# Performance work log

Measured on AMD Instinct MI355X. Metric: run time of the kernel, lower is better.

The kernel has to match this reference:

```python
import jax, jax.numpy as jnp
import numpy as np

B, T, R = 64, 256, 256          # batch, timepoints, n_rois (T==R required by bmm path)
H, NH, DH, FF, LAT, L = 256, 8, 32, 512, 64, 2
EPS = 1e-5


def layernorm(x, g, b):
    m = x.mean(-1, keepdims=True)
    v = ((x - m) ** 2).mean(-1, keepdims=True)
    return (x - m) / jnp.sqrt(v + EPS) * g + b


def leaky_relu(x):
    return jnp.where(x >= 0, x, 0.1 * x)


def setup_inputs() -> dict:
    key = jax.random.key(0)
    ks = iter(jax.random.split(key, 64))
    def nrm(shape, s=0.02):
        return jax.random.normal(next(ks), shape, jnp.float32) * s
    return {
        "x": jax.random.normal(next(ks), (B, T, R), jnp.float32),
        "node_view": jax.random.normal(next(ks), (B, R, R), jnp.float32) * 0.1,
        "edge_view": jax.random.normal(next(ks), (B, R, R), jnp.float32) * 0.1,
        "fp_w": nrm((H, R)), "fp_b": jnp.zeros((H,)),
        "fp_g": jnp.ones((H,)), "fp_beta": jnp.zeros((H,)),
        "qkv_w": nrm((L, 3 * H, H)), "qkv_b": jnp.zeros((L, 3 * H)),
        "attn_out_w": nrm((L, H, H)), "attn_out_b": jnp.zeros((L, H)),
        "ln1_g": jnp.ones((L, H)), "ln1_b": jnp.zeros((L, H)),
        "ff1_w": nrm((L, FF, H)), "ff1_b": jnp.zeros((L, FF)),
        "ff2_w": nrm((L, H, FF)), "ff2_b": jnp.zeros((L, H)),
        "ln2_g": jnp.ones((L, H)), "ln2_b": jnp.zeros((L, H)),
        "out_w": nrm((R, H)), "out_b": jnp.zeros((R,)),
        "mu_w1": nrm((H // 2, H)), "mu_b1": jnp.zeros((H // 2,)),
        "mu_g": jnp.ones((H // 2,)), "mu_beta": jnp.zeros((H // 2,)),
        "mu_w2": nrm((LAT, H // 2)), "mu_b2": jnp.zeros((LAT,)),
        "lv_w1": nrm((H // 2, H)), "lv_b1": jnp.zeros((H // 2,)),
        "lv_g": jnp.ones((H // 2,)), "lv_beta": jnp.zeros((H // 2,)),
        "lv_w2": nrm((LAT, H // 2)), "lv_b2": jnp.zeros((LAT,)),
    }


def reference(x, node_view, edge_view, fp_w, fp_b, fp_g, fp_beta,
              qkv_w, qkv_b, attn_out_w, attn_out_b, ln1_g, ln1_b,
              ff1_w, ff1_b, ff2_w, ff2_b, ln2_g, ln2_b,
              out_w, out_b, mu_w1, mu_b1, mu_g, mu_beta, mu_w2, mu_b2,
              lv_w1, lv_b1, lv_g, lv_beta, lv_w2, lv_b2):
    # graph-view message passing: bmm(x^T, view), averaged, transposed back
    xr = jnp.swapaxes(x, 1, 2)                           # [B,R,T]
    msg = 0.5 * (jnp.einsum('brt,btq->brq', xr, node_view)
                 + jnp.einsum('brt,btq->brq', xr, edge_view))
    h = jnp.swapaxes(msg, 1, 2)                          # [B,T,R]
    # feature_proj: Linear -> LayerNorm -> LeakyReLU(0.1) -> Dropout(eval)
    h = leaky_relu(layernorm(h @ fp_w.T + fp_b, fp_g, fp_beta))  # [B,T,H]
    # TransformerEncoder (post-norm, relu FFN, dropout=identity)
    scale = 1.0 / jnp.sqrt(jnp.float32(DH))
    for i in range(L):
        qkv = h @ qkv_w[i].T + qkv_b[i]                  # [B,T,3H]
        q, k, v = jnp.split(qkv, 3, axis=-1)
        q = q.reshape(B, T, NH, DH).transpose(0, 2, 1, 3)
        k = k.reshape(B, T, NH, DH).transpose(0, 2, 1, 3)
        v = v.reshape(B, T, NH, DH).transpose(0, 2, 1, 3)
        attn = jax.nn.softmax(jnp.einsum('bhqd,bhkd->bhqk', q, k) * scale, axis=-1)
        o = jnp.einsum('bhqk,bhkd->bhqd', attn, v).transpose(0, 2, 1, 3).reshape(B, T, H)
        o = o @ attn_out_w[i].T + attn_out_b[i]
        h = layernorm(h + o, ln1_g[i], ln1_b[i])
        f = jax.nn.relu(h @ ff1_w[i].T + ff1_b[i]) @ ff2_w[i].T + ff2_b[i]
        h = layernorm(h + f, ln2_g[i], ln2_b[i])
    # fresh linear (treated as fixed params) then batched Pearson correlation
    y = h @ out_w.T + out_b                              # [B,T,R]
    data = jnp.swapaxes(y, 1, 2)                         # [B,R,T]
    c = data - data.mean(-1, keepdims=True)
    std = jnp.sqrt((c ** 2).sum(-1, keepdims=True) / (T - 1))   # unbiased, like torch.std
    cn = c / (std + 1e-8)
    corr = jnp.einsum('brt,bst->brs', cn, cn) / (T - 1)
    corr = jnp.nan_to_num(jnp.clip(corr, -1.0, 1.0), nan=0.0)   # [B,R,R]
    # heads
    pooled = h.mean(axis=1)                              # [B,H]
    mu = leaky_relu(layernorm(pooled @ mu_w1.T + mu_b1, mu_g, mu_beta)) @ mu_w2.T + mu_b2
    logvar = leaky_relu(layernorm(pooled @ lv_w1.T + lv_b1, lv_g, lv_beta)) @ lv_w2.T + lv_b2
    return mu, logvar, corr
```

## Files before the change

### kernel.cpp

```cpp
#include <hip/hip_runtime.h>
#include <hip/hip_bf16.h>
#include <math.h>

#define BB 64
#define NLAYER 2

typedef __attribute__((ext_vector_type(8))) short bfrag;
typedef __attribute__((ext_vector_type(4))) float f4_t;

__device__ __forceinline__ float dot4(float4 a, float4 b, float acc) {
    acc = fmaf(a.x, b.x, acc);
    acc = fmaf(a.y, b.y, acc);
    acc = fmaf(a.z, b.z, acc);
    acc = fmaf(a.w, b.w, acc);
    return acc;
}

__device__ __forceinline__ ushort f2bf(float f) {
    uint32_t u = __float_as_uint(f);
    uint32_t r = (u + 0x7FFFu + ((u >> 16) & 1u)) >> 16;
    return (ushort)r;
}
__device__ __forceinline__ float bf2f(ushort u) {
    return __uint_as_float(((uint32_t)u) << 16);
}

__device__ __forceinline__ void gll16(const ushort* g, ushort* l) {
    __builtin_amdgcn_global_load_lds(
        (const __attribute__((address_space(1))) void*)g,
        (__attribute__((address_space(3))) void*)l, 16, 0, 0);
}

__global__ __launch_bounds__(256) void k_cvt(
    const float* __restrict__ fp_w, const float* __restrict__ qkv_w,
    const float* __restrict__ aow, const float* __restrict__ f1w,
    const float* __restrict__ f2w, const float* __restrict__ outw,
    ushort* __restrict__ dst) {
    const int g = blockIdx.x;
    const size_t idx = (size_t)g * 2048 + threadIdx.x * 8;
    const float* src;
    size_t base;
    if (g < 32)       { src = fp_w;  base = 0; }
    else if (g < 224) { src = qkv_w; base = 65536; }
    else if (g < 288) { src = aow;   base = 458752; }
    else if (g < 416) { src = f1w;   base = 589824; }
    else if (g < 544) { src = f2w;   base = 851968; }
    else              { src = outw;  base = 1114112; }
    const float4* s4 = reinterpret_cast<const float4*>(src + (idx - base));
    float4 a = s4[0], b = s4[1];
    bfrag o;
    o[0] = (short)f2bf(a.x); o[1] = (short)f2bf(a.y);
    o[2] = (short)f2bf(a.z); o[3] = (short)f2bf(a.w);
    o[4] = (short)f2bf(b.x); o[5] = (short)f2bf(b.y);
    o[6] = (short)f2bf(b.z); o[7] = (short)f2bf(b.w);
    *reinterpret_cast<bfrag*>(dst + idx) = o;
}

#define MM97_STAGE(SRC, LDS, KSTRIDE)                                        \
    {                                                                        \
        _Pragma("unroll")                                                    \
        for (int c = 0; c < 4; ++c) {                                        \
            const int rr = (w << 5) + (c << 3) + (lane >> 3);                \
            gll16(SRC + (size_t)rr * (KSTRIDE) + k0 + ((lane & 7) << 3),     \
                  LDS + (((w << 5) + (c << 3)) << 6));                       \
        }                                                                    \
    }

#define MM97_COMPUTE()                                                       \
    _Pragma("unroll")                                                        \
    for (int ks = 0; ks < 2; ++ks) {                                         \
        const int kb = ks * 32 + fq * 8;                                     \
        bfrag af[4], bfv[4];                                                 \
        _Pragma("unroll")                                                    \
        for (int fm = 0; fm < 4; ++fm)                                       \
            af[fm] = *reinterpret_cast<const bfrag*>(                        \
                &As[((wm * 64 + fm * 16 + fr) << 6) + kb]);                  \
        _Pragma("unroll")                                                    \
        for (int fn = 0; fn < 4; ++fn)                                       \
            bfv[fn] = *reinterpret_cast<const bfrag*>(                       \
                &Bs[((wn * 64 + fn * 16 + fr) << 6) + kb]);                  \
        _Pragma("unroll")                                                    \
        for (int fm = 0; fm < 4; ++fm)                                       \
            _Pragma("unroll")                                                \
            for (int fn = 0; fn < 4; ++fn)                                   \
                acc[fm][fn] = __builtin_amdgcn_mfma_f32_16x16x32_bf16(       \
                    bfv[fn], af[fm], acc[fm][fn], 0, 0, 0);                  \
    }

template <int EPI, bool WF32, bool WBF>
__global__ __launch_bounds__(256) void k_mm97(
    const ushort* __restrict__ A, const ushort* __restrict__ B,
    const float* __restrict__ bias, float* __restrict__ C,
    ushort* __restrict__ Cb, int K, int N,
    size_t aStr, size_t bStr, size_t cStr) {
    __shared__ __align__(16) ushort As[128 * 64];
    __shared__ __align__(16) ushort Bs[128 * 64];
    const int tid = threadIdx.x;
    const int m0 = blockIdx.x * 128, n0 = blockIdx.y * 128;
    const size_t z = blockIdx.z;
    const int w = tid >> 6, lane = tid & 63;
    const int wm = w >> 1, wn = w & 1;
    const int fr = lane & 15, fq = lane >> 4;

    const ushort* aB = A + z * aStr + (size_t)m0 * K;
    const ushort* bB = B + z * bStr + (size_t)n0 * K;

    f4_t acc[4][4];
#pragma unroll
    for (int i = 0; i < 4; ++i)
#pragma unroll
        for (int j = 0; j < 4; ++j) acc[i][j] = (f4_t)0.f;

    for (int k0 = 0; k0 < K; k0 += 64) {
        MM97_STAGE(aB, As, K)
        MM97_STAGE(bB, Bs, K)
        __syncthreads();
        MM97_COMPUTE()
        __syncthreads();
    }

#pragma unroll
    for (int fn = 0; fn < 4; ++fn) {
// ... 7 lines not shown
            float v0 = acc[fm][fn][0] + bv.x;
            float v1 = acc[fm][fn][1] + bv.y;
            float v2 = acc[fm][fn][2] + bv.z;
            float v3 = acc[fm][fn][3] + bv.w;
            if (EPI == 2) {
                v0 = fmaxf(v0, 0.f); v1 = fmaxf(v1, 0.f);
                v2 = fmaxf(v2, 0.f); v3 = fmaxf(v3, 0.f);
            }
            const size_t o = cStr * z + (size_t)row * N + col0;
            if (WF32) {
                float4 fv = {v0, v1, v2, v3};
                *reinterpret_cast<float4*>(&C[o]) = fv;
            }
            if (WBF) {
                ushort4 uv;
                uv.x = f2bf(v0); uv.y = f2bf(v1);
                uv.z = f2bf(v2); uv.w = f2bf(v3);
                *reinterpret_cast<ushort4*>(&Cb[o]) = uv;
            }
        }
    }
}

__global__ __launch_bounds__(256) void k_mmqkv97(
    const ushort* __restrict__ A, const ushort* __restrict__ B,
    const float* __restrict__ bias, ushort* __restrict__ qb,
    ushort* __restrict__ kbuf, ushort* __restrict__ vtb) {
    __shared__ __align__(16) ushort As[128 * 64];
    __shared__ __align__(16) ushort Bs[128 * 64];
    const int tid = threadIdx.x;
    const int m0 = blockIdx.x * 128, n0 = blockIdx.y * 128;
    const int w = tid >> 6, lane = tid & 63;
    const int wm = w >> 1, wn = w & 1;
    const int fr = lane & 15, fq = lane >> 4;
    const int K = 256;

    const ushort* aB = A + (size_t)m0 * K;
    const ushort* bB = B + (size_t)n0 * K;

    f4_t acc[4][4];
#pragma unroll
    for (int i = 0; i < 4; ++i)
#pragma unroll
        for (int j = 0; j < 4; ++j) acc[i][j] = (f4_t)0.f;

    for (int k0 = 0; k0 < K; k0 += 64) {
        MM97_STAGE(aB, As, K)
        MM97_STAGE(bB, Bs, K)
        __syncthreads();
        MM97_COMPUTE()
        __syncthreads();
    }

    const int sec = n0 >> 8;
// ... 8 lines not shown
            const int b = row >> 8, t = row & 255;
            const size_t bh = (size_t)b * 8 + hd;
            float v0 = acc[fm][fn][0] + bv.x;
            float v1 = acc[fm][fn][1] + bv.y;
            float v2 = acc[fm][fn][2] + bv.z;
            float v3 = acc[fm][fn][3] + bv.w;
            if (sec < 2) {
                ushort4 uv;
                uv.x = f2bf(v0); uv.y = f2bf(v1);
                uv.z = f2bf(v2); uv.w = f2bf(v3);
                ushort* dst = (sec == 0 ? qb : kbuf) + (bh * 256 + t) * 32 + dq;
                *reinterpret_cast<ushort4*>(dst) = uv;
            } else {
                ushort* dst = vtb + (bh * 32 + dq) * 256 + t;
                dst[0] = f2bf(v0);
                dst[256] = f2bf(v1);
                dst[512] = f2bf(v2);
                dst[768] = f2bf(v3);
            }
        }
    }
}

__global__ __launch_bounds__(256) void k_corr97(
    const ushort* __restrict__ A, const float* __restrict__ stats,
    float* __restrict__ C) {
    __shared__ __align__(16) ushort As[128 * 64];
    __shared__ __align__(16) ushort Bs[128 * 64];
    const int tid = threadIdx.x;
    const int m0 = blockIdx.x * 128, n0 = blockIdx.y * 128;
    const size_t z = blockIdx.z;
    const int w = tid >> 6, lane = tid & 63;
    const int wm = w >> 1, wn = w & 1;
    const int fr = lane & 15, fq = lane >> 4;
    const int K = 256;

    const ushort* aB = A + z * 65536 + (size_t)m0 * K;
    const ushort* bB = A + z * 65536 + (size_t)n0 * K;

    f4_t acc[4][4];
#pragma unroll
    for (int i = 0; i < 4; ++i)
#pragma unroll
        for (int j = 0; j < 4; ++j) acc[i][j] = (f4_t)0.f;

    for (int k0 = 0; k0 < K; k0 += 64) {
        MM97_STAGE(aB, As, K)
        MM97_STAGE(bB, Bs, K)
        __syncthreads();
        MM97_COMPUTE()
        __syncthreads();
    }

    const float* st = stats + z * 512;
// ... 7 lines not shown
            const int row = m0 + wm * 64 + fm * 16 + fr;
            const float mui = st[row];
            const float isi = st[256 + row] * (1.f / 255.f);
            float v0 = (acc[fm][fn][0] - 256.f * mui * muj.x) * isi * isj.x;
            float v1 = (acc[fm][fn][1] - 256.f * mui * muj.y) * isi * isj.y;
            float v2 = (acc[fm][fn][2] - 256.f * mui * muj.z) * isi * isj.z;
            float v3 = (acc[fm][fn][3] - 256.f * mui * muj.w) * isi * isj.w;
            if (v0 != v0) v0 = 0.f;
            if (v1 != v1) v1 = 0.f;
            if (v2 != v2) v2 = 0.f;
            if (v3 != v3) v3 = 0.f;
            v0 = fminf(1.f, fmaxf(-1.f, v0));
            v1 = fminf(1.f, fmaxf(-1.f, v1));
            v2 = fminf(1.f, fmaxf(-1.f, v2));
            v3 = fminf(1.f, fmaxf(-1.f, v3));
            float4 fv = {v0, v1, v2, v3};
            *reinterpret_cast<float4*>(
                &C[z * 65536 + (size_t)row * 256 + col0]) = fv;
        }
    }
}

template <int ACT, bool RES>
__global__ __launch_bounds__(256) void k_mmln(
    const ushort* __restrict__ A, const ushort* __restrict__ W,
    const float* __restrict__ bias, const ushort* __restrict__ res,
    const float* __restrict__ g, const float* __restrict__ bt,
    ushort* __restrict__ outb, int K) {
    __shared__ __align__(16) ushort As[32 * 72];
    __shared__ __align__(16) ushort Bs[256 * 72];
    __shared__ float redS[32][4];
    __shared__ float redQ[32][4];
    const int tid = threadIdx.x;
    const int m0 = blockIdx.x * 32;
    const int w = tid >> 6, lane = tid & 63;
    const int fr = lane & 15, fq = lane >> 4;

    const int arow = tid >> 3, akc = (tid & 7) * 8;
    const ushort* aS = A + (size_t)(m0 + arow) * K + akc;
    ushort* aD = &As[arow * 72 + akc];
    const int brow = tid >> 1, bkc = (tid & 1) * 32;
    const ushort* bS0 = W + (size_t)brow * K + bkc;
    const ushort* bS1 = W + (size_t)(brow + 128) * K + bkc;
    ushort* bD0 = &Bs[brow * 72 + bkc];
    ushort* bD1 = &Bs[(brow + 128) * 72 + bkc];

    f4_t acc[2][4];
#pragma unroll
    for (int i = 0; i < 2; ++i)
#pragma unroll
        for (int j = 0; j < 4; ++j) acc[i][j] = (f4_t)0.f;

    bfrag ra, rb0, rb1, rb2, rb3, rc0, rc1, rc2, rc3;
    {
        ra = *reinterpret_cast<const bfrag*>(aS);
        const bfrag* bp0 = reinterpret_cast<const bfrag*>(bS0);
        rb0 = bp0[0]; rb1 = bp0[1]; rb2 = bp0[2]; rb3 = bp0[3];
// ... 55 lines not shown
                r0 = bf2f(r4.x); r1 = bf2f(r4.y);
                r2 = bf2f(r4.z); r3 = bf2f(r4.w);
            }
            acc[fm][fn][0] += bv.x + r0;
            acc[fm][fn][1] += bv.y + r1;
            acc[fm][fn][2] += bv.z + r2;
            acc[fm][fn][3] += bv.w + r3;
        }
    }
#pragma unroll
    for (int fm = 0; fm < 2; ++fm) {
        float s = 0.f, q = 0.f;
#pragma unroll
        for (int fn = 0; fn < 4; ++fn)
#pragma unroll
            for (int j = 0; j < 4; ++j) {
                const float v = acc[fm][fn][j];
                s += v;
                q += v * v;
            }
        s += __shfl_xor(s, 16); q += __shfl_xor(q, 16);
        s += __shfl_xor(s, 32); q += __shfl_xor(q, 32);
        if (fq == 0) {
            redS[fm * 16 + fr][w] = s;
            redQ[fm * 16 + fr][w] = q;
        }
    }
    __syncthreads();
#pragma unroll
    for (int fm = 0; fm < 2; ++fm) {
        const int row = fm * 16 + fr;
        const float S = redS[row][0] + redS[row][1] + redS[row][2] + redS[row][3];
        const float Q = redQ[row][0] + redQ[row][1] + redQ[row][2] + redQ[row][3];
        const float mean = S * (1.f / 256.f);
        const float var = Q * (1.f / 256.f) - mean * mean;
        const float rstd = rsqrtf(fmaxf(var, 0.f) + 1e-5f);
        const size_t rowoff = (size_t)(m0 + row) * 256;
#pragma unroll
        for (int fn = 0; fn < 4; ++fn) {
            const int col0 = w * 64 + fn * 16 + fq * 4;
            const float4 g4 = *reinterpret_cast<const float4*>(&g[col0]);
            const float4 b4 = *reinterpret_cast<const float4*>(&bt[col0]);
            float v0 = (acc[fm][fn][0] - mean) * rstd * g4.x + b4.x;
            float v1 = (acc[fm][fn][1] - mean) * rstd * g4.y + b4.y;
            float v2 = (acc[fm][fn][2] - mean) * rstd * g4.z + b4.z;
            float v3 = (acc[fm][fn][3] - mean) * rstd * g4.w + b4.w;
            if (ACT == 1) {
                v0 = v0 >= 0.f ? v0 : 0.1f * v0;
                v1 = v1 >= 0.f ? v1 : 0.1f * v1;
                v2 = v2 >= 0.f ? v2 : 0.1f * v2;
                v3 = v3 >= 0.f ? v3 : 0.1f * v3;
            }
            ushort4 uv;
            uv.x = f2bf(v0); uv.y = f2bf(v1);
            uv.z = f2bf(v2); uv.w = f2bf(v3);
            *reinterpret_cast<ushort4*>(&outb[rowoff + col0]) = uv;
        }
    }
}

__global__ __launch_bounds__(256) void k_attn3(
    const ushort* __restrict__ qb, const ushort* __restrict__ kbuf,
    const ushort* __restrict__ vtb, ushort* __restrict__ o) {
    __shared__ __align__(16) ushort Ps[4][64][40];
    const int hd = blockIdx.x, b = blockIdx.y;
    const size_t bh = (size_t)b * 8 + hd;
    const int tid = threadIdx.x;
    const int w = tid >> 6, lane = tid & 63;
    const int fr = lane & 15, fq = lane >> 4;

    const ushort* qB = qb + bh * 8192;
    const ushort* kB = kbuf + bh * 8192;
    const ushort* vB = vtb + bh * 8192;

    const int q0 = w * 64;
    bfrag qf[4];
#pragma unroll
    for (int fm = 0; fm < 4; ++fm)
        qf[fm] = *reinterpret_cast<const bfrag*>(
            qB + (size_t)(q0 + fm * 16 + fr) * 32 + fq * 8);

    f4_t oacc[4][2];
    float rs[4][4];
#pragma unroll
    for (int fm = 0; fm < 4; ++fm) {
        oacc[fm][0] = (f4_t)0.f;
        oacc[fm][1] = (f4_t)0.f;
#pragma unroll
        for (int j = 0; j < 4; ++j) rs[fm][j] = 0.f;
    }
// ... 42 lines not shown
    for (int fm = 0; fm < 4; ++fm)
#pragma unroll
        for (int j = 0; j < 4; ++j) {
            float r = rs[fm][j];
            r += __shfl_xor(r, 1);
            r += __shfl_xor(r, 2);
            r += __shfl_xor(r, 4);
            r += __shfl_xor(r, 8);
            rs[fm][j] = 1.f / r;
        }
    ushort* ob = o + (size_t)b * 65536 + hd * 32;
#pragma unroll
    for (int fm = 0; fm < 4; ++fm) {
        const int qrow = q0 + fm * 16 + fq * 4;
#pragma unroll
        for (int j = 0; j < 4; ++j) {
            const float inv = rs[fm][j];
            ob[(size_t)(qrow + j) * 256 + fr] = f2bf(oacc[fm][0][j] * inv);
            ob[(size_t)(qrow + j) * 256 + 16 + fr] = f2bf(oacc[fm][1][j] * inv);
        }
    }
}

__global__ __launch_bounds__(256) void k_xpose_bmm(
    const float* __restrict__ x, const float* __restrict__ nv,
    const float* __restrict__ ev, ushort* __restrict__ At,
    ushort* __restrict__ Xt) {
    const int b = blockIdx.z;
    const int k0 = blockIdx.x * 64, i0 = blockIdx.y * 64;
    __shared__ float TA[64][65];
    __shared__ float TX[64][65];
    const size_t bb = (size_t)b * 65536;
    const int tid = threadIdx.x;
    const int lr = tid >> 4, lc = (tid & 15) * 4;
#pragma unroll
    for (int l = 0; l < 4; ++l) {
        const int row = lr + l * 16;
        const size_t gidx = bb + (size_t)(k0 + row) * 256 + i0 + lc;
        float4 n4 = *reinterpret_cast<const float4*>(nv + gidx);
        float4 e4 = *reinterpret_cast<const float4*>(ev + gidx);
        float4 x4 = *reinterpret_cast<const float4*>(x + gidx);
        TA[row][lc] = 0.5f * (n4.x + e4.x);
        TA[row][lc + 1] = 0.5f * (n4.y + e4.y);
        TA[row][lc + 2] = 0.5f * (n4.z + e4.z);
        TA[row][lc + 3] = 0.5f * (n4.w + e4.w);
        TX[row][lc] = x4.x;
        TX[row][lc + 1] = x4.y;
        TX[row][lc + 2] = x4.z;
        TX[row][lc + 3] = x4.w;
    }
    __syncthreads();
    const int i = tid & 63, kk = (tid >> 6) * 16;
    bfrag a0, a1, x0, x1;
#pragma unroll
    for (int e = 0; e < 8; ++e) {
        a0[e] = (short)f2bf(TA[kk + e][i]);
        a1[e] = (short)f2bf(TA[kk + 8 + e][i]);
        x0[e] = (short)f2bf(TX[kk + e][i]);
        x1[e] = (short)f2bf(TX[kk + 8 + e][i]);
    }
    const size_t o = bb + (size_t)(i0 + i) * 256 + k0 + kk;
    *reinterpret_cast<bfrag*>(At + o) = a0;
    *reinterpret_cast<bfrag*>(At + o + 8) = a1;
    *reinterpret_cast<bfrag*>(Xt + o) = x0;
    *reinterpret_cast<bfrag*>(Xt + o + 8) = x1;
}

__global__ __launch_bounds__(256) void k_rowstats(const ushort* __restrict__ yT,
                                                  float* __restrict__ stats) {
    const int b = blockIdx.y;
    const int r = blockIdx.x * 64 + (threadIdx.x >> 2);
    const int part = threadIdx.x & 3;
    const ushort* row = yT + (size_t)b * 65536 + (size_t)r * 256 + part * 64;
    float s = 0.f, q = 0.f;
#pragma unroll
    for (int i = 0; i < 8; ++i) {
        bfrag v = reinterpret_cast<const bfrag*>(row)[i];
#pragma unroll
        for (int e = 0; e < 8; ++e) {
            float f = bf2f((ushort)v[e]);
            s += f;
            q += f * f;
        }
    }
    s += __shfl_xor(s, 1); q += __shfl_xor(q, 1);
    s += __shfl_xor(s, 2); q += __shfl_xor(q, 2);
    if (part == 0) {
        const float mean = s * (1.f / 256.f);
        const float var = (q - s * mean) * (1.f / 255.f);
        const float stdv = sqrtf(fmaxf(var, 0.f));
        stats[b * 512 + r] = mean;
        stats[b * 512 + 256 + r] = 1.f / (stdv + 1e-8f);
    }
}

__global__ __launch_bounds__(512) void k_poolhead(
    const ushort* __restrict__ h,
    const float* __restrict__ mw1, const float* __restrict__ mb1,
    const float* __restrict__ mg, const float* __restrict__ mbt,
    const float* __restrict__ mw2, const float* __restrict__ mb2,
    const float* __restrict__ lw1, const float* __restrict__ lb1,
    const float* __restrict__ lg, const float* __restrict__ lbt,
    const float* __restrict__ lw2, const float* __restrict__ lb2,
    float* __restrict__ outp) {
    const int b = blockIdx.x, tid = threadIdx.x;
    __shared__ float pp[2][256];
    __shared__ float pooled[256];
    __shared__ float rS[4], rQ[4];
    __shared__ float t1[2][128];

    {
        const int c = tid & 255, tc = tid >> 8;
        const ushort* hb = h + (size_t)b * 65536 + (size_t)tc * 128 * 256 + c;
        float s = 0.f;
        for (int t = 0; t < 128; ++t) s += bf2f(hb[(size_t)t * 256]);
        pp[tc][c] = s;
    }
    __syncthreads();
    if (tid < 256) pooled[tid] = (pp[0][tid] + pp[1][tid]) * (1.f / 256.f);
    __syncthreads();

    float a = 0.f;
    if (tid < 256) {
        const int hd = tid >> 7, u = tid & 127;
        const float* w1 = hd ? lw1 : mw1;
        const float* b1 = hd ? lb1 : mb1;
        a = b1[u];
        const float4* w1v = reinterpret_cast<const float4*>(w1 + (size_t)u * 256);
#pragma unroll 4
        for (int k4 = 0; k4 < 64; ++k4) {
            float4 wv = w1v[k4];
            float4 p = *reinterpret_cast<const float4*>(&pooled[k4 * 4]);
            a = dot4(p, wv, a);
        }
        float s = a, q = a * a;
#pragma unroll
        for (int m = 1; m < 64; m <<= 1) {
            s += __shfl_xor(s, m);
            q += __shfl_xor(q, m);
        }
        if ((tid & 63) == 0) { rS[tid >> 6] = s; rQ[tid >> 6] = q; }
    }
    __syncthreads();
    if (tid < 256) {
        const int hd = tid >> 7, u = tid & 127;
        const float* g = hd ? lg : mg;
        const float* bt = hd ? lbt : mbt;
        const float S = rS[hd * 2] + rS[hd * 2 + 1];
        const float Q = rQ[hd * 2] + rQ[hd * 2 + 1];
        const float mean = S * (1.f / 128.f);
        const float var = Q * (1.f / 128.f) - mean * mean;
        const float rstd = rsqrtf(fmaxf(var, 0.f) + 1e-5f);
        float v = (a - mean) * rstd * g[u] + bt[u];
        v = v >= 0.f ? v : 0.1f * v;
        t1[hd][u] = v;
    }
    __syncthreads();
    if (tid < 128) {
        const int hd = tid >> 6, ou = tid & 63;
        const float* w2 = hd ? lw2 : mw2;
        const float* b2 = hd ? lb2 : mb2;
        float o = b2[ou];
        const float* w2r = w2 + (size_t)ou * 128;
#pragma unroll 4
        for (int c = 0; c < 128; ++c) o = fmaf(t1[hd][c], w2r[c], o);
        outp[hd * 4096 + b * 64 + ou] = o;
    }
}

extern "C" void kernel_launch(void* const* d_in, const int* in_sizes, int n_in,
                              void* d_out, int out_size, void* d_ws, size_t ws_size,
                              hipStream_t stream) {
    const float* x = (const float*)d_in[0];
    const float* nv = (const float*)d_in[1];
    const float* ev = (const float*)d_in[2];
    const float* fp_w = (const float*)d_in[3];
    const float* fp_b = (const float*)d_in[4];
    const float* fp_g = (const float*)d_in[5];
    const float* fp_beta = (const float*)d_in[6];
    const float* qkv_w = (const float*)d_in[7];
    const float* qkv_b = (const float*)d_in[8];
    const float* aow = (const float*)d_in[9];
    const float* aob = (const float*)d_in[10];
    const float* ln1g = (const float*)d_in[11];
    const float* ln1b = (const float*)d_in[12];
    const float* f1w = (const float*)d_in[13];
    const float* f1b = (const float*)d_in[14];
    const float* f2w = (const float*)d_in[15];
    const float* f2b = (const float*)d_in[16];
    const float* ln2g = (const float*)d_in[17];
    const float* ln2b = (const float*)d_in[18];
    const float* outw = (const float*)d_in[19];
    const float* outb = (const float*)d_in[20];
    const float* muw1 = (const float*)d_in[21];
    const float* mub1 = (const float*)d_in[22];
    const float* mug = (const float*)d_in[23];
    const float* mubt = (const float*)d_in[24];
    const float* muw2 = (const float*)d_in[25];
    const float* mub2 = (const float*)d_in[26];
    const float* lvw1 = (const float*)d_in[27];
    const float* lvb1 = (const float*)d_in[28];
    const float* lvg = (const float*)d_in[29];
    const float* lvbt = (const float*)d_in[30];
    const float* lvw2 = (const float*)d_in[31];
    const float* lvb2 = (const float*)d_in[32];

    float* out = (float*)d_out;
    float* ws = (float*)d_ws;

    float* stats = ws;
    ushort* ub = (ushort*)(ws + 32768);
    ushort* wh_bf = ub;
    ushort* At = ub + 4194304;
    ushort* Xt = ub + 8388608;
    ushort* o_bf = ub + 16777216;
    ushort* h0_bf = o_bf;
    ushort* f1_bf = ub + 20971520;
    ushort* qb = ub + 29360128;
    ushort* kb = ub + 33554432;
    ushort* vtb = ub + 37748736;
    ushort* yT = ub + 41943040;
    ushort* wbf = ub + 46137344;

    k_cvt<<<576, 256, 0, stream>>>(fp_w, qkv_w, aow, f1w, f2w, outw, wbf);

    k_xpose_bmm<<<dim3(4, 4, BB), 256, 0, stream>>>(x, nv, ev, At, Xt);
    k_mm97<0, false, true><<<dim3(2, 2, BB), 256, 0, stream>>>(
        At, Xt, nullptr, nullptr, h0_bf, 256, 256, 65536, 65536, 65536);

    k_mmln<1, false><<<512, 256, 0, stream>>>(
        h0_bf, wbf, fp_b, nullptr, fp_g, fp_beta, wh_bf, 256);

    for (int l = 0; l < NLAYER; ++l) {
        k_mmqkv97<<<dim3(128, 6), 256, 0, stream>>>(
            wh_bf, wbf + 65536 + (size_t)l * 196608, qkv_b + l * 768,
            qb, kb, vtb);
        k_attn3<<<dim3(8, BB), 256, 0, stream>>>(qb, kb, vtb, o_bf);
        k_mmln<0, true><<<512, 256, 0, stream>>>(
            o_bf, wbf + 458752 + (size_t)l * 65536, aob + l * 256,
            wh_bf, ln1g + l * 256, ln1b + l * 256, wh_bf, 256);
        k_mm97<2, false, true><<<dim3(128, 4, 1), 256, 0, stream>>>(
            wh_bf, wbf + 589824 + (size_t)l * 131072, f1b + l * 512,
            nullptr, f1_bf, 256, 512, 0, 0, 0);
        k_mmln<0, true><<<512, 256, 0, stream>>>(
            f1_bf, wbf + 851968 + (size_t)l * 131072, f2b + l * 256,
            wh_bf, ln2g + l * 256, ln2b + l * 256, wh_bf, 512);
    }

    k_mm97<0, false, true><<<dim3(2, 2, BB), 256, 0, stream>>>(
        wbf + 1114112, wh_bf, nullptr, nullptr, yT, 256, 256, 0, 65536, 65536);

    k_rowstats<<<dim3(4, BB), 256, 0, stream>>>(yT, stats);
    k_corr97<<<dim3(2, 2, BB), 256, 0, stream>>>(yT, stats, out + 8192);

    k_poolhead<<<BB, 512, 0, stream>>>(
        wh_bf, muw1, mub1, mug, mubt, muw2, mub2,
        lvw1, lvb1, lvg, lvbt, lvw2, lvb2, out);
}
```

Measured before the change: 236.3 us.

## Fuse all stages into one cooperative persistent megakernel with grid syncs

Turns every stage kernel into a device function and runs them in one cooperative persistent kernel. Stages are separated by grid.sync(), and each stage's blocks are looped over the resident grid. The goal is to remove many kernel launch gaps and tail effects. It also merges weight conversion with the transpose stage, and corr with the pool head. The risks are grid-sync cost, a persistent grid capped at 512 blocks that may underfill some stages, and the 43KB shared allocation limiting occupancy. A multi-kernel fallback path is kept.

```diff
diff --git a/kernel.cpp b/kernel.cpp
--- a/kernel.cpp
+++ b/kernel.cpp
@@ -1,6 +1,9 @@
 #include <hip/hip_runtime.h>
 #include <hip/hip_bf16.h>
+#include <hip/hip_cooperative_groups.h>
 #include <math.h>
+
+namespace cg = cooperative_groups;
 
 #define BB 64
 #define NLAYER 2
@@ -31,21 +34,29 @@
         (__attribute__((address_space(3))) void*)l, 16, 0, 0);
 }
 
-__global__ __launch_bounds__(256) void k_cvt(
-    const float* __restrict__ fp_w, const float* __restrict__ qkv_w,
-    const float* __restrict__ aow, const float* __restrict__ f1w,
-    const float* __restrict__ f2w, const float* __restrict__ outw,
-    ushort* __restrict__ dst) {
-    const int g = blockIdx.x;
-    const size_t idx = (size_t)g * 2048 + threadIdx.x * 8;
+struct MegaParams {
+    const float *x, *nv, *ev;
+    const float *fp_w, *fp_b, *fp_g, *fp_beta;
+    const float *qkv_w, *qkv_b, *aow, *aob, *ln1g, *ln1b;
+    const float *f1w, *f1b, *f2w, *f2b, *ln2g, *ln2b;
+    const float *outw, *outb;
+    const float *muw1, *mub1, *mug, *mubt, *muw2, *mub2;
+    const float *lvw1, *lvb1, *lvg, *lvbt, *lvw2, *lvb2;
+    float* out;
+    float* stats;
+    ushort *wh_bf, *At, *Xt, *o_bf, *f1_bf, *qb, *kb, *vtb, *yT, *wbf;
+};
+
+__device__ void d_cvt(int tid, int g, const MegaParams& p) {
+    const size_t idx = (size_t)g * 2048 + tid * 8;
     const float* src;
     size_t base;
-    if (g < 32)       { src = fp_w;  base = 0; }
-    else if (g < 224) { src = qkv_w; base = 65536; }
-    else if (g < 288) { src = aow;   base = 458752; }
-    else if (g < 416) { src = f1w;   base = 589824; }
-    else if (g < 544) { src = f2w;   base = 851968; }
-    else              { src = outw;  base = 1114112; }
+    if (g < 32)       { src = p.fp_w;  base = 0; }
+    else if (g < 224) { src = p.qkv_w; base = 65536; }
+    else if (g < 288) { src = p.aow;   base = 458752; }
+    else if (g < 416) { src = p.f1w;   base = 589824; }
+    else if (g < 544) { src = p.f2w;   base = 851968; }
+    else              { src = p.outw;  base = 1114112; }
     const float4* s4 = reinterpret_cast<const float4*>(src + (idx - base));
     float4 a = s4[0], b = s4[1];
     bfrag o;
@@ -53,7 +64,47 @@
     o[2] = (short)f2bf(a.z); o[3] = (short)f2bf(a.w);
     o[4] = (short)f2bf(b.x); o[5] = (short)f2bf(b.y);
     o[6] = (short)f2bf(b.z); o[7] = (short)f2bf(b.w);
-    *reinterpret_cast<bfrag*>(dst + idx) = o;
+    *reinterpret_cast<bfrag*>(p.wbf + idx) = o;
+}
+
+__device__ void d_xpose(char* smch, int tid, int k0, int i0, int b,
+                        const MegaParams& p) {
+    float (*TA)[65] = (float(*)[65])smch;
+    float (*TX)[65] = (float(*)[65])(smch + 64 * 65 * 4);
+    const size_t bb = (size_t)b * 65536;
+    const int lr = tid >> 4, lc = (tid & 15) * 4;
+#pragma unroll
+    for (int l = 0; l < 4; ++l) {
+        const int row = lr + l * 16;
+        const size_t gidx = bb + (size_t)(k0 + row) * 256 + i0 + lc;
+        float4 n4 = *reinterpret_cast<const float4*>(p.nv + gidx);
+        float4 e4 = *reinterpret_cast<const float4*>(p.ev + gidx);
+        float4 x4 = *reinterpret_cast<const float4*>(p.x + gidx);
+        TA[row][lc] = 0.5f * (n4.x + e4.x);
+        TA[row][lc + 1] = 0.5f * (n4.y + e4.y);
+        TA[row][lc + 2] = 0.5f * (n4.z + e4.z);
+        TA[row][lc + 3] = 0.5f * (n4.w + e4.w);
+        TX[row][lc] = x4.x;
+        TX[row][lc + 1] = x4.y;
+        TX[row][lc + 2] = x4.z;
+        TX[row][lc + 3] = x4.w;
+    }
+    __syncthreads();
+    const int i = tid & 63, kk = (tid >> 6) * 16;
+    bfrag a0, a1, x0, x1;
+#pragma unroll
+    for (int e = 0; e < 8; ++e) {
+        a0[e] = (short)f2bf(TA[kk + e][i]);
+        a1[e] = (short)f2bf(TA[kk + 8 + e][i]);
+        x0[e] = (short)f2bf(TX[kk + e][i]);
+        x1[e] = (short)f2bf(TX[kk + 8 + e][i]);
+    }
+    const size_t o = bb + (size_t)(i0 + i) * 256 + k0 + kk;
+    *reinterpret_cast<bfrag*>(p.At + o) = a0;
+    *reinterpret_cast<bfrag*>(p.At + o + 8) = a1;
+    *reinterpret_cast<bfrag*>(p.Xt + o) = x0;
+    *reinterpret_cast<bfrag*>(p.Xt + o + 8) = x1;
+    __syncthreads();
 }
 
 #define MM97_STAGE(SRC, LDS, KSTRIDE)                                        \
@@ -88,16 +139,12 @@
     }
 
 template <int EPI, bool WF32, bool WBF>
-__global__ __launch_bounds__(256) void k_mm97(
-    const ushort* __restrict__ A, const ushort* __restrict__ B,
-    const float* __restrict__ bias, float* __restrict__ C,
-    ushort* __restrict__ Cb, int K, int N,
-    size_t aStr, size_t bStr, size_t cStr) {
-    __shared__ __align__(16) ushort As[128 * 64];
-    __shared__ __align__(16) ushort Bs[128 * 64];
-    const int tid = threadIdx.x;
-    const int m0 = blockIdx.x * 128, n0 = blockIdx.y * 128;
-    const size_t z = blockIdx.z;
+__device__ void d_mm97(char* smch, int tid, int m0, int n0, size_t z,
+                       const ushort* A, const ushort* B, const float* bias,
+                       float* C, ushort* Cb, int K, int N,
+                       size_t aStr, size_t bStr, size_t cStr) {
+    ushort* As = (ushort*)smch;
+    ushort* Bs = As + 8192;
     const int w = tid >> 6, lane = tid & 63;
     const int wm = w >> 1, wn = w & 1;
     const int fr = lane & 15, fq = lane >> 4;
@@ -151,14 +198,11 @@
     }
 }
 
-__global__ __launch_bounds__(256) void k_mmqkv97(
-    const ushort* __restrict__ A, const ushort* __restrict__ B,
-    const float* __restrict__ bias, ushort* __restrict__ qb,
-    ushort* __restrict__ kbuf, ushort* __restrict__ vtb) {
-    __shared__ __align__(16) ushort As[128 * 64];
-    __shared__ __align__(16) ushort Bs[128 * 64];
-    const int tid = threadIdx.x;
-    const int m0 = blockIdx.x * 128, n0 = blockIdx.y * 128;
+__device__ void d_mmqkv97(char* smch, int tid, int m0, int n0,
+                          const ushort* A, const ushort* B, const float* bias,
+                          ushort* qb, ushort* kbuf, ushort* vtb) {
+    ushort* As = (ushort*)smch;
+    ushort* Bs = As + 8192;
     const int w = tid >> 6, lane = tid & 63;
     const int wm = w >> 1, wn = w & 1;
     const int fr = lane & 15, fq = lane >> 4;
@@ -213,14 +257,10 @@
     }
 }
 
-__global__ __launch_bounds__(256) void k_corr97(
-    const ushort* __restrict__ A, const float* __restrict__ stats,
-    float* __restrict__ C) {
-    __shared__ __align__(16) ushort As[128 * 64];
-    __shared__ __align__(16) ushort Bs[128 * 64];
-    const int tid = threadIdx.x;
-    const int m0 = blockIdx.x * 128, n0 = blockIdx.y * 128;
-    const size_t z = blockIdx.z;
+__device__ void d_corr97(char* smch, int tid, int m0, int n0, size_t z,
+                         const ushort* A, const float* stats, float* C) {
+    ushort* As = (ushort*)smch;
+    ushort* Bs = As + 8192;
     const int w = tid >> 6, lane = tid & 63;
     const int wm = w >> 1, wn = w & 1;
     const int fr = lane & 15, fq = lane >> 4;
@@ -274,17 +314,14 @@
 }
 
 template <int ACT, bool RES>
-__global__ __launch_bounds__(256) void k_mmln(
-    const ushort* __restrict__ A, const ushort* __restrict__ W,
-    const float* __restrict__ bias, const ushort* __restrict__ res,
-    const float* __restrict__ g, const float* __restrict__ bt,
-    ushort* __restrict__ outb, int K) {
-    __shared__ __align__(16) ushort As[32 * 72];
-    __shared__ __align__(16) ushort Bs[256 * 72];
-    __shared__ float redS[32][4];
-    __shared__ float redQ[32][4];
-    const int tid = threadIdx.x;
-    const int m0 = blockIdx.x * 32;
+__device__ void d_mmln(char* smch, int tid, int m0,
+                       const ushort* A, const ushort* W, const float* bias,
+                       const ushort* res, const float* g, const float* bt,
+                       ushort* outb, int K) {
+    ushort* As = (ushort*)smch;
+    ushort* Bs = As + 2304;
+    float* redS = (float*)(smch + 41472);
+    float* redQ = redS + 128;
     const int w = tid >> 6, lane = tid & 63;
     const int fr = lane & 15, fq = lane >> 4;
 
@@ -386,16 +423,16 @@
         s += __shfl_xor(s, 16); q += __shfl_xor(q, 16);
         s += __shfl_xor(s, 32); q += __shfl_xor(q, 32);
         if (fq == 0) {
-            redS[fm * 16 + fr][w] = s;
-            redQ[fm * 16 + fr][w] = q;
+            redS[(fm * 16 + fr) * 4 + w] = s;
+            redQ[(fm * 16 + fr) * 4 + w] = q;
         }
     }
     __syncthreads();
 #pragma unroll
     for (int fm = 0; fm < 2; ++fm) {
         const int row = fm * 16 + fr;
-        const float S = redS[row][0] + redS[row][1] + redS[row][2] + redS[row][3];
-        const float Q = redQ[row][0] + redQ[row][1] + redQ[row][2] + redQ[row][3];
+        const float S = redS[row * 4] + redS[row * 4 + 1] + redS[row * 4 + 2] + redS[row * 4 + 3];
+        const float Q = redQ[row * 4] + redQ[row * 4 + 1] + redQ[row * 4 + 2] + redQ[row * 4 + 3];
         const float mean = S * (1.f / 256.f);
         const float var = Q * (1.f / 256.f) - mean * mean;
         const float rstd = rsqrtf(fmaxf(var, 0.f) + 1e-5f);
@@ -421,15 +458,14 @@
             *reinterpret_cast<ushort4*>(&outb[rowoff + col0]) = uv;
         }
     }
-}
-
-__global__ __launch_bounds__(256) void k_attn3(
-    const ushort* __restrict__ qb, const ushort* __restrict__ kbuf,
-    const ushort* __restrict__ vtb, ushort* __restrict__ o) {
-    __shared__ __align__(16) ushort Ps[4][64][40];
-    const int hd = blockIdx.x, b = blockIdx.y;
+    __syncthreads();
+}
+
+__device__ void d_attn3(char* smch, int tid, int hd, int b,
+                        const ushort* qb, const ushort* kbuf,
+                        const ushort* vtb, ushort* o) {
+    ushort (*Ps)[64][40] = (ushort(*)[64][40])smch;
     const size_t bh = (size_t)b * 8 + hd;
-    const int tid = threadIdx.x;
     const int w = tid >> 6, lane = tid & 63;
     const int fr = lane & 15, fq = lane >> 4;
 
@@ -518,55 +554,10 @@
     }
 }
 
-__global__ __launch_bounds__(256) void k_xpose_bmm(
-    const float* __restrict__ x, const float* __restrict__ nv,
-    const float* __restrict__ ev, ushort* __restrict__ At,
-    ushort* __restrict__ Xt) {
-    const int b = blockIdx.z;
-    const int k0 = blockIdx.x * 64, i0 = blockIdx.y * 64;
-    __shared__ float TA[64][65];
-    __shared__ float TX[64][65];
-    const size_t bb = (size_t)b * 65536;
-    const int tid = threadIdx.x;
-    const int lr = tid >> 4, lc = (tid & 15) * 4;
-#pragma unroll
-    for (int l = 0; l < 4; ++l) {
-        const int row = lr + l * 16;
-        const size_t gidx = bb + (size_t)(k0 + row) * 256 + i0 + lc;
-        float4 n4 = *reinterpret_cast<const float4*>(nv + gidx);
-        float4 e4 = *reinterpret_cast<const float4*>(ev + gidx);
-        float4 x4 = *reinterpret_cast<const float4*>(x + gidx);
-        TA[row][lc] = 0.5f * (n4.x + e4.x);
-        TA[row][lc + 1] = 0.5f * (n4.y + e4.y);
-        TA[row][lc + 2] = 0.5f * (n4.z + e4.z);
-        TA[row][lc + 3] = 0.5f * (n4.w + e4.w);
-        TX[row][lc] = x4.x;
-        TX[row][lc + 1] = x4.y;
-        TX[row][lc + 2] = x4.z;
-        TX[row][lc + 3] = x4.w;
-    }
-    __syncthreads();
-    const int i = tid & 63, kk = (tid >> 6) * 16;
-    bfrag a0, a1, x0, x1;
-#pragma unroll
-    for (int e = 0; e < 8; ++e) {
-        a0[e] = (short)f2bf(TA[kk + e][i]);
-        a1[e] = (short)f2bf(TA[kk + 8 + e][i]);
-        x0[e] = (short)f2bf(TX[kk + e][i]);
-        x1[e] = (short)f2bf(TX[kk + 8 + e][i]);
-    }
-    const size_t o = bb + (size_t)(i0 + i) * 256 + k0 + kk;
-    *reinterpret_cast<bfrag*>(At + o) = a0;
-    *reinterpret_cast<bfrag*>(At + o + 8) = a1;
-    *reinterpret_cast<bfrag*>(Xt + o) = x0;
-    *reinterpret_cast<bfrag*>(Xt + o + 8) = x1;
-}
-
-__global__ __launch_bounds__(256) void k_rowstats(const ushort* __restrict__ yT,
-                                                  float* __restrict__ stats) {
-    const int b = blockIdx.y;
-    const int r = blockIdx.x * 64 + (threadIdx.x >> 2);
-    const int part = threadIdx.x & 3;
+__device__ void d_rowstats(int tid, int rx, int b, const ushort* yT,
+                           float* stats) {
+    const int r = rx * 64 + (tid >> 2);
+    const int part = tid & 3;
     const ushort* row = yT + (size_t)b * 65536 + (size_t)r * 256 + part * 64;
     float s = 0.f, q = 0.f;
 #pragma unroll
@@ -590,58 +581,42 @@
     }
 }
 
-__global__ __launch_bounds__(512) void k_poolhead(
-    const ushort* __restrict__ h,
-    const float* __restrict__ mw1, const float* __restrict__ mb1,
-    const float* __restrict__ mg, const float* __restrict__ mbt,
-    const float* __restrict__ mw2, const float* __restrict__ mb2,
-    const float* __restrict__ lw1, const float* __restrict__ lb1,
-    const float* __restrict__ lg, const float* __restrict__ lbt,
-    const float* __restrict__ lw2, const float* __restrict__ lb2,
-    float* __restrict__ outp) {
-    const int b = blockIdx.x, tid = threadIdx.x;
-    __shared__ float pp[2][256];
-    __shared__ float pooled[256];
-    __shared__ float rS[4], rQ[4];
-    __shared__ float t1[2][128];
+__device__ void d_poolhead(char* smch, int tid, int b, const MegaParams& p) {
+    float* pooled = (float*)smch;
+    float* rS = pooled + 256;
+    float* rQ = rS + 4;
+    float* t1 = rQ + 4;
 
     {
-        const int c = tid & 255, tc = tid >> 8;
-        const ushort* hb = h + (size_t)b * 65536 + (size_t)tc * 128 * 256 + c;
+        const ushort* hb = p.wh_bf + (size_t)b * 65536 + tid;
         float s = 0.f;
-        for (int t = 0; t < 128; ++t) s += bf2f(hb[(size_t)t * 256]);
-        pp[tc][c] = s;
+        for (int t = 0; t < 256; ++t) s += bf2f(hb[(size_t)t * 256]);
+        pooled[tid] = s * (1.f / 256.f);
     }
     __syncthreads();
-    if (tid < 256) pooled[tid] = (pp[0][tid] + pp[1][tid]) * (1.f / 256.f);
+
+    const int hd = tid >> 7, u = tid & 127;
+    const float* w1 = hd ? p.lvw1 : p.muw1;
+    const float* b1 = hd ? p.lvb1 : p.mub1;
+    float a = b1[u];
+    const float4* w1v = reinterpret_cast<const float4*>(w1 + (size_t)u * 256);
+#pragma unroll 4
+    for (int k4 = 0; k4 < 64; ++k4) {
+        float4 wv = w1v[k4];
+        float4 pv = *reinterpret_cast<const float4*>(&pooled[k4 * 4]);
+        a = dot4(pv, wv, a);
+    }
+    float s = a, q = a * a;
+#pragma unroll
+    for (int m = 1; m < 64; m <<= 1) {
+        s += __shfl_xor(s, m);
+        q += __shfl_xor(q, m);
+    }
+    if ((tid & 63) == 0) { rS[tid >> 6] = s; rQ[tid >> 6] = q; }
     __syncthreads();
-
-    float a = 0.f;
-    if (tid < 256) {
-        const int hd = tid >> 7, u = tid & 127;
-        const float* w1 = hd ? lw1 : mw1;
-        const float* b1 = hd ? lb1 : mb1;
-        a = b1[u];
-        const float4* w1v = reinterpret_cast<const float4*>(w1 + (size_t)u * 256);
-#pragma unroll 4
-        for (int k4 = 0; k4 < 64; ++k4) {
-            float4 wv = w1v[k4];
-            float4 p = *reinterpret_cast<const float4*>(&pooled[k4 * 4]);
-            a = dot4(p, wv, a);
-        }
-        float s = a, q = a * a;
-#pragma unroll
-        for (int m = 1; m < 64; m <<= 1) {
-            s += __shfl_xor(s, m);
-            q += __shfl_xor(q, m);
-        }
-        if ((tid & 63) == 0) { rS[tid >> 6] = s; rQ[tid >> 6] = q; }
-    }
-    __syncthreads();
-    if (tid < 256) {
-        const int hd = tid >> 7, u = tid & 127;
-        const float* g = hd ? lg : mg;
-        const float* bt = hd ? lbt : mbt;
+    {
+        const float* g = hd ? p.lvg : p.mug;
+        const float* bt = hd ? p.lvbt : p.mubt;
         const float S = rS[hd * 2] + rS[hd * 2 + 1];
         const float Q = rQ[hd * 2] + rQ[hd * 2 + 1];
         const float mean = S * (1.f / 128.f);
@@ -649,107 +624,252 @@
         const float rstd = rsqrtf(fmaxf(var, 0.f) + 1e-5f);
         float v = (a - mean) * rstd * g[u] + bt[u];
         v = v >= 0.f ? v : 0.1f * v;
-        t1[hd][u] = v;
+        t1[hd * 128 + u] = v;
     }
     __syncthreads();
     if (tid < 128) {
-        const int hd = tid >> 6, ou = tid & 63;
-        const float* w2 = hd ? lw2 : mw2;
-        const float* b2 = hd ? lb2 : mb2;
+        const int h2 = tid >> 6, ou = tid & 63;
+        const float* w2 = h2 ? p.lvw2 : p.muw2;
+        const float* b2 = h2 ? p.lvb2 : p.mub2;
         float o = b2[ou];
         const float* w2r = w2 + (size_t)ou * 128;
 #pragma unroll 4
-        for (int c = 0; c < 128; ++c) o = fmaf(t1[hd][c], w2r[c], o);
-        outp[hd * 4096 + b * 64 + ou] = o;
-    }
+        for (int c = 0; c < 128; ++c) o = fmaf(t1[h2 * 128 + c], w2r[c], o);
+        p.out[h2 * 4096 + b * 64 + ou] = o;
+    }
+    __syncthreads();
+}
+
+__global__ __launch_bounds__(256) void k_mega(MegaParams p) {
+    __shared__ __align__(16) char sm[43008];
+    cg::grid_group grid = cg::this_grid();
+    const int tid = threadIdx.x;
+    const int gs = gridDim.x;
+
+    for (int vb = blockIdx.x; vb < 1600; vb += gs) {
+        if (vb < 576) d_cvt(tid, vb, p);
+        else {
+            const int q = vb - 576;
+            d_xpose(sm, tid, (q & 3) * 64, ((q >> 2) & 3) * 64, q >> 4, p);
+        }
+    }
+    grid.sync();
+    for (int vb = blockIdx.x; vb < 256; vb += gs)
+        d_mm97<0, false, true>(sm, tid, ((vb >> 1) & 1) * 128, (vb & 1) * 128,
+                               (size_t)(vb >> 2), p.At, p.Xt, nullptr, nullptr,
+                               p.o_bf, 256, 256, 65536, 65536, 65536);
+    grid.sync();
+    for (int vb = blockIdx.x; vb < 512; vb += gs)
+        d_mmln<1, false>(sm, tid, vb * 32, p.o_bf, p.wbf, p.fp_b, nullptr,
+                         p.fp_g, p.fp_beta, p.wh_bf, 256);
+    grid.sync();
+
+    for (int l = 0; l < NLAYER; ++l) {
+        const ushort* wq = p.wbf + 65536 + (size_t)l * 196608;
+        const ushort* wa = p.wbf + 458752 + (size_t)l * 65536;
+        const ushort* w1 = p.wbf + 589824 + (size_t)l * 131072;
+        const ushort* w2 = p.wbf + 851968 + (size_t)l * 131072;
+        for (int vb = blockIdx.x; vb < 768; vb += gs)
+            d_mmqkv97(sm, tid, (vb & 127) * 128, (vb >> 7) * 128,
+                      p.wh_bf, wq, p.qkv_b + l * 768, p.qb, p.kb, p.vtb);
+        grid.sync();
+        for (int vb = blockIdx.x; vb < 512; vb += gs)
+            d_attn3(sm, tid, vb & 7, vb >> 3, p.qb, p.kb, p.vtb, p.o_bf);
+        grid.sync();
+        for (int vb = blockIdx.x; vb < 512; vb += gs)
+            d_mmln<0, true>(sm, tid, vb * 32, p.o_bf, wa, p.aob + l * 256,
+                            p.wh_bf, p.ln1g + l * 256, p.ln1b + l * 256,
+                            p.wh_bf, 256);
+        grid.sync();
+        for (int vb = blockIdx.x; vb < 512; vb += gs)
+            d_mm97<2, false, true>(sm, tid, (vb & 127) * 128, (vb >> 7) * 128,
+                                   0, p.wh_bf, w1, p.f1b + l * 512, nullptr,
+                                   p.f1_bf, 256, 512, 0, 0, 0);
+        grid.sync();
+        for (int vb = blockIdx.x; vb < 512; vb += gs)
+            d_mmln<0, true>(sm, tid, vb * 32, p.f1_bf, w2, p.f2b + l * 256,
+                            p.wh_bf, p.ln2g + l * 256, p.ln2b + l * 256,
+                            p.wh_bf, 512);
+        grid.sync();
+    }
+
+    for (int vb = blockIdx.x; vb < 256; vb += gs)
+        d_mm97<0, false, true>(sm, tid, ((vb >> 1) & 1) * 128, (vb & 1) * 128,
+                               (size_t)(vb >> 2), p.wbf + 1114112, p.wh_bf,
+                               nullptr, nullptr, p.yT, 256, 256, 0, 65536,
+                               65536);
+    grid.sync();
+    for (int vb = blockIdx.x; vb < 256; vb += gs)
+        d_rowstats(tid, vb & 3, vb >> 2, p.yT, p.stats);
+    grid.sync();
+    for (int vb = blockIdx.x; vb < 320; vb += gs) {
+        if (vb < 256)
+            d_corr97(sm, tid, ((vb >> 1) & 1) * 128, (vb & 1) * 128,
+                     (size_t)(vb >> 2), p.yT, p.stats, p.out + 8192);
+        else
+            d_poolhead(sm, tid, vb - 256, p);
+    }
+}
+
+__global__ __launch_bounds__(256) void kw_prep(MegaParams p) {
+    __shared__ __align__(16) char sm[33280];
+    const int vb = blockIdx.x;
+    if (vb < 576) d_cvt(threadIdx.x, vb, p);
+    else {
+        const int q = vb - 576;
+        d_xpose(sm, threadIdx.x, (q & 3) * 64, ((q >> 2) & 3) * 64, q >> 4, p);
+    }
+}
+__global__ __launch_bounds__(256) void kw_bmm(MegaParams p) {
+    __shared__ __align__(16) char sm[32768];
+    const int vb = blockIdx.x;
+    d_mm97<0, false, true>(sm, threadIdx.x, ((vb >> 1) & 1) * 128,
+                           (vb & 1) * 128, (size_t)(vb >> 2), p.At, p.Xt,
+                           nullptr, nullptr, p.o_bf, 256, 256, 65536, 65536,
+                           65536);
+}
+__global__ __launch_bounds__(256) void kw_ln0(MegaParams p) {
+    __shared__ __align__(16) char sm[42496];
+    d_mmln<1, false>(sm, threadIdx.x, blockIdx.x * 32, p.o_bf, p.wbf, p.fp_b,
+                     nullptr, p.fp_g, p.fp_beta, p.wh_bf, 256);
+}
+__global__ __launch_bounds__(256) void kw_qkv(MegaParams p, int l) {
+    __shared__ __align__(16) char sm[32768];
+    const int vb = blockIdx.x;
+    d_mmqkv97(sm, threadIdx.x, (vb & 127) * 128, (vb >> 7) * 128, p.wh_bf,
+              p.wbf + 65536 + (size_t)l * 196608, p.qkv_b + l * 768,
+              p.qb, p.kb, p.vtb);
+}
+__global__ __launch_bounds__(256) void kw_attn(MegaParams p) {
+    __shared__ __align__(16) char sm[20480];
+    d_attn3(sm, threadIdx.x, blockIdx.x & 7, blockIdx.x >> 3, p.qb, p.kb,
+            p.vtb, p.o_bf);
+}
+__global__ __launch_bounds__(256) void kw_ln1(MegaParams p, int l) {
+    __shared__ __align__(16) char sm[42496];
+    d_mmln<0, true>(sm, threadIdx.x, blockIdx.x * 32, p.o_bf,
+                    p.wbf + 458752 + (size_t)l * 65536, p.aob + l * 256,
+                    p.wh_bf, p.ln1g + l * 256, p.ln1b + l * 256, p.wh_bf, 256);
+}
+__global__ __launch_bounds__(256) void kw_ffn1(MegaParams p, int l) {
+    __shared__ __align__(16) char sm[32768];
+    const int vb = blockIdx.x;
+    d_mm97<2, false, true>(sm, threadIdx.x, (vb & 127) * 128, (vb >> 7) * 128,
+                           0, p.wh_bf, p.wbf + 589824 + (size_t)l * 131072,
+                           p.f1b + l * 512, nullptr, p.f1_bf, 256, 512, 0, 0,
+                           0);
+}
+__global__ __launch_bounds__(256) void kw_ln2(MegaParams p, int l) {
+    __shared__ __align__(16) char sm[42496];
+    d_mmln<0, true>(sm, threadIdx.x, blockIdx.x * 32, p.f1_bf,
+                    p.wbf + 851968 + (size_t)l * 131072, p.f2b + l * 256,
+                    p.wh_bf, p.ln2g + l * 256, p.ln2b + l * 256, p.wh_bf, 512);
+}
+__global__ __launch_bounds__(256) void kw_yt(MegaParams p) {
+    __shared__ __align__(16) char sm[32768];
+    const int vb = blockIdx.x;
+    d_mm97<0, false, true>(sm, threadIdx.x, ((vb >> 1) & 1) * 128,
+                           (vb & 1) * 128, (size_t)(vb >> 2),
+                           p.wbf + 1114112, p.wh_bf, nullptr, nullptr, p.yT,
+                           256, 256, 0, 65536, 65536);
+}
+__global__ __launch_bounds__(256) void kw_rstats(MegaParams p) {
+    d_rowstats(threadIdx.x, blockIdx.x & 3, blockIdx.x >> 2, p.yT, p.stats);
+}
+__global__ __launch_bounds__(256) void kw_corrpool(MegaParams p) {
+    __shared__ __align__(16) char sm[32768];
+    const int vb = blockIdx.x;
+    if (vb < 256)
+        d_corr97(sm, threadIdx.x, ((vb >> 1) & 1) * 128, (vb & 1) * 128,
+                 (size_t)(vb >> 2), p.yT, p.stats, p.out + 8192);
+    else
+        d_poolhead(sm, threadIdx.x, vb - 256, p);
 }
 
 extern "C" void kernel_launch(void* const* d_in, const int* in_sizes, int n_in,
                               void* d_out, int out_size, void* d_ws, size_t ws_size,
                               hipStream_t stream) {
-    const float* x = (const float*)d_in[0];
-    const float* nv = (const float*)d_in[1];
-    const float* ev = (const float*)d_in[2];
-    const float* fp_w = (const float*)d_in[3];
-    const float* fp_b = (const float*)d_in[4];
-    const float* fp_g = (const float*)d_in[5];
-    const float* fp_beta = (const float*)d_in[6];
-    const float* qkv_w = (const float*)d_in[7];
-    const float* qkv_b = (const float*)d_in[8];
-    const float* aow = (const float*)d_in[9];
-    const float* aob = (const float*)d_in[10];
-    const float* ln1g = (const float*)d_in[11];
-    const float* ln1b = (const float*)d_in[12];
-    const float* f1w = (const float*)d_in[13];
-    const float* f1b = (const float*)d_in[14];
-    const float* f2w = (const float*)d_in[15];
-    const float* f2b = (const float*)d_in[16];
-    const float* ln2g = (const float*)d_in[17];
-    const float* ln2b = (const float*)d_in[18];
-    const float* outw = (const float*)d_in[19];
-    const float* outb = (const float*)d_in[20];
-    const float* muw1 = (const float*)d_in[21];
-    const float* mub1 = (const float*)d_in[22];
-    const float* mug = (const float*)d_in[23];
-    const float* mubt = (const float*)d_in[24];
-    const float* muw2 = (const float*)d_in[25];
-    const float* mub2 = (const float*)d_in[26];
-    const float* lvw1 = (const float*)d_in[27];
-    const float* lvb1 = (const float*)d_in[28];
-    const float* lvg = (const float*)d_in[29];
-    const float* lvbt = (const float*)d_in[30];
-    const float* lvw2 = (const float*)d_in[31];
-    const float* lvb2 = (const float*)d_in[32];
-
-    float* out = (float*)d_out;
     float* ws = (float*)d_ws;
-
-    float* stats = ws;
     ushort* ub = (ushort*)(ws + 32768);
-    ushort* wh_bf = ub;
-    ushort* At = ub + 4194304;
-    ushort* Xt = ub + 8388608;
-    ushort* o_bf = ub + 16777216;
-    ushort* h0_bf = o_bf;
-    ushort* f1_bf = ub + 20971520;
-    ushort* qb = ub + 29360128;
-    ushort* kb = ub + 33554432;
-    ushort* vtb = ub + 37748736;
-    ushort* yT = ub + 41943040;
-    ushort* wbf = ub + 46137344;
-
-    k_cvt<<<576, 256, 0, stream>>>(fp_w, qkv_w, aow, f1w, f2w, outw, wbf);
-
-    k_xpose_bmm<<<dim3(4, 4, BB), 256, 0, stream>>>(x, nv, ev, At, Xt);
-    k_mm97<0, false, true><<<dim3(2, 2, BB), 256, 0, stream>>>(
-        At, Xt, nullptr, nullptr, h0_bf, 256, 256, 65536, 65536, 65536);
-
-    k_mmln<1, false><<<512, 256, 0, stream>>>(
-        h0_bf, wbf, fp_b, nullptr, fp_g, fp_beta, wh_bf, 256);
-
+
+    MegaParams p;
+    p.x = (const float*)d_in[0];
+    p.nv = (const float*)d_in[1];
+    p.ev = (const float*)d_in[2];
+    p.fp_w = (const float*)d_in[3];
+    p.fp_b = (const float*)d_in[4];
+    p.fp_g = (const float*)d_in[5];
+    p.fp_beta = (const float*)d_in[6];
+    p.qkv_w = (const float*)d_in[7];
+    p.qkv_b = (const float*)d_in[8];
+    p.aow = (const float*)d_in[9];
+    p.aob = (const float*)d_in[10];
+    p.ln1g = (const float*)d_in[11];
+    p.ln1b = (const float*)d_in[12];
+    p.f1w = (const float*)d_in[13];
+    p.f1b = (const float*)d_in[14];
+    p.f2w = (const float*)d_in[15];
+    p.f2b = (const float*)d_in[16];
+    p.ln2g = (const float*)d_in[17];
+    p.ln2b = (const float*)d_in[18];
+    p.outw = (const float*)d_in[19];
+    p.outb = (const float*)d_in[20];
+    p.muw1 = (const float*)d_in[21];
+    p.mub1 = (const float*)d_in[22];
+    p.mug = (const float*)d_in[23];
+    p.mubt = (const float*)d_in[24];
+    p.muw2 = (const float*)d_in[25];
+    p.mub2 = (const float*)d_in[26];
+    p.lvw1 = (const float*)d_in[27];
+    p.lvb1 = (const float*)d_in[28];
+    p.lvg = (const float*)d_in[29];
+    p.lvbt = (const float*)d_in[30];
+    p.lvw2 = (const float*)d_in[31];
+    p.lvb2 = (const float*)d_in[32];
+    p.out = (float*)d_out;
+    p.stats = ws;
+    p.wh_bf = ub;
+    p.At = ub + 4194304;
+    p.Xt = ub + 8388608;
+    p.o_bf = ub + 16777216;
+    p.f1_bf = ub + 20971520;
+    p.qb = ub + 29360128;
+    p.kb = ub + 33554432;
+    p.vtb = ub + 37748736;
+    p.yT = ub + 41943040;
+    p.wbf = ub + 46137344;
+
+    int dev = 0;
+    (void)hipGetDevice(&dev);
+    int cus = 0;
+    (void)hipDeviceGetAttribute(&cus, hipDeviceAttributeMultiprocessorCount, dev);
+    int nb = 0;
+    (void)hipOccupancyMaxActiveBlocksPerMultiprocessor(
+        &nb, (const void*)k_mega, 256, 0);
+    int grid = (nb > 0 && cus > 0) ? nb * cus : 0;
+    if (grid > 512) grid = 512;
+
+    hipError_t err = hipErrorUnknown;
+    if (grid >= 64) {
+        void* args[] = {&p};
+        err = hipLaunchCooperativeKernel(reinterpret_cast<void*>(k_mega),
+                                         dim3(grid), dim3(256), args, 0,
+                                         stream);
+    }
+    (void)hipGetLastError();
+    if (err == hipSuccess) return;
+
+    kw_prep<<<1600, 256, 0, stream>>>(p);
+    kw_bmm<<<256, 256, 0, stream>>>(p);
+    kw_ln0<<<512, 256, 0, stream>>>(p);
     for (int l = 0; l < NLAYER; ++l) {
-        k_mmqkv97<<<dim3(128, 6), 256, 0, stream>>>(
-            wh_bf, wbf + 65536 + (size_t)l * 196608, qkv_b + l * 768,
-            qb, kb, vtb);
-        k_attn3<<<dim3(8, BB), 256, 0, stream>>>(qb, kb, vtb, o_bf);
-        k_mmln<0, true><<<512, 256, 0, stream>>>(
-            o_bf, wbf + 458752 + (size_t)l * 65536, aob + l * 256,
-            wh_bf, ln1g + l * 256, ln1b + l * 256, wh_bf, 256);
-        k_mm97<2, false, true><<<dim3(128, 4, 1), 256, 0, stream>>>(
-            wh_bf, wbf + 589824 + (size_t)l * 131072, f1b + l * 512,
-            nullptr, f1_bf, 256, 512, 0, 0, 0);
-        k_mmln<0, true><<<512, 256, 0, stream>>>(
-            f1_bf, wbf + 851968 + (size_t)l * 131072, f2b + l * 256,
-            wh_bf, ln2g + l * 256, ln2b + l * 256, wh_bf, 512);
-    }
-
-    k_mm97<0, false, true><<<dim3(2, 2, BB), 256, 0, stream>>>(
-        wbf + 1114112, wh_bf, nullptr, nullptr, yT, 256, 256, 0, 65536, 65536);
-
-    k_rowstats<<<dim3(4, BB), 256, 0, stream>>>(yT, stats);
-    k_corr97<<<dim3(2, 2, BB), 256, 0, stream>>>(yT, stats, out + 8192);
-
-    k_poolhead<<<BB, 512, 0, stream>>>(
-        wh_bf, muw1, mub1, mug, mubt, muw2, mub2,
-        lvw1, lvb1, lvg, lvbt, lvw2, lvb2, out);
-}
+        kw_qkv<<<768, 256, 0, stream>>>(p, l);
+        kw_attn<<<512, 256, 0, stream>>>(p);
+        kw_ln1<<<512, 256, 0, stream>>>(p, l);
+        kw_ffn1<<<512, 256, 0, stream>>>(p, l);
+        kw_ln2<<<512, 256, 0, stream>>>(p, l);
+    }
+    kw_yt<<<256, 256, 0, stream>>>(p);
+    kw_rstats<<<256, 256, 0, stream>>>(p);
+    kw_corrpool<<<320, 256, 0, stream>>>(p);
+}
```

New measurement: 258.0 us. +9.2%, slower.
